# Kernel tuning notes

Measured on AMD Instinct MI355X. Metric: run time of the kernel, lower is better.

The kernel has to match this reference:

```python
import jax, jax.numpy as jnp
import numpy as np

COMMITMENT_COST = 0.25


def setup_inputs() -> dict:
    key = jax.random.key(0)
    k1, k2 = jax.random.split(key)
    B, S, D, K = 8, 4096, 256, 1024
    inputs = jax.random.normal(k1, (B, S, D), dtype=jnp.float32)
    attention_mask = jnp.ones((B, S), dtype=jnp.float32)
    codebook = jax.random.normal(k2, (K, D), dtype=jnp.float32)
    return {"inputs": inputs, "attention_mask": attention_mask, "codebook": codebook}


def reference(inputs, attention_mask, codebook):
    # Inference-mode forward of VectorQuantizer (no EMA update / init / revival).
    B, S, D = inputs.shape
    z = inputs.astype(jnp.float32).reshape(-1, D)          # (N, D)
    m = attention_mask.reshape(-1).astype(jnp.float32)     # (N,)

    cb = codebook.astype(jnp.float32)                      # (K, D)
    # squared L2 distances: ||z||^2 - 2 z e^T + ||e||^2
    dist = (jnp.sum(z * z, axis=-1, keepdims=True)
            - 2.0 * jnp.matmul(z, cb.T)
            + jnp.sum(cb * cb, axis=-1)[None, :])          # (N, K)
    idx = jnp.argmin(dist, axis=-1)                        # (N,)
    q = cb[idx]                                            # (N, D) codebook lookup

    n_valid = jnp.sum(m)
    # mse over valid tokens (elementwise mean, matching F.mse_loss on flat_valid)
    diff = z - jax.lax.stop_gradient(q)
    commitment = jnp.sum(m[:, None] * diff * diff) / (n_valid * D)
    vq_loss = COMMITMENT_COST * commitment

    # straight-through estimator; invalid positions zeroed (as in torch scatter)
    q_ste = z + jax.lax.stop_gradient(q - z)
    quantized = (q_ste * m[:, None]).reshape(B, S, D)
    indices = jnp.where(m > 0, idx, 0).reshape(B, S)
    return quantized, vq_loss, indices
```

## Files before the change

kernel.cpp:

```cpp
#include <hip/hip_runtime.h>
#include <cstdint>

typedef short bf16x8 __attribute__((ext_vector_type(8)));
typedef float f32x16 __attribute__((ext_vector_type(16)));

#define TOK    64
#define CH     64
#define NCH    16
#define BUFW   16384
#define MAXC   32

__device__ __forceinline__ unsigned short f2bf(float f) {
  unsigned u = __float_as_uint(f);
  return (unsigned short)((u + 0x7FFFu + ((u >> 16) & 1u)) >> 16);
}
__device__ __forceinline__ uint4 pack8(float4 a, float4 b) {
  uint4 u;
  u.x = (unsigned)f2bf(a.x) | ((unsigned)f2bf(a.y) << 16);
  u.y = (unsigned)f2bf(a.z) | ((unsigned)f2bf(a.w) << 16);
  u.z = (unsigned)f2bf(b.x) | ((unsigned)f2bf(b.y) << 16);
  u.w = (unsigned)f2bf(b.z) | ((unsigned)f2bf(b.w) << 16);
  return u;
}
__device__ __forceinline__ void gload16(const unsigned short* g, unsigned short* l) {
  __builtin_amdgcn_global_load_lds(
      (const __attribute__((address_space(1))) unsigned int*)(const void*)g,
      (__attribute__((address_space(3))) unsigned int*)(void*)l, 16, 0, 0);
}

__global__ __launch_bounds__(256) void vq_prep(const float* __restrict__ cb,
                                               unsigned short* __restrict__ cb_bf,
                                               float* __restrict__ ee,
                                               float* __restrict__ acc2,
                                               int* __restrict__ done_ctr, int K) {
  if (blockIdx.x == 0 && threadIdx.x == 0) {
    acc2[0] = 0.f; acc2[1] = 0.f; *done_ctr = 0;
  }
  int wave = threadIdx.x >> 6, lane = threadIdx.x & 63;
  int k = blockIdx.x * 4 + wave;
  if (k >= K) return;
  float4 v = *reinterpret_cast<const float4*>(cb + (size_t)k * 256 + lane * 4);
  float s = v.x * v.x + v.y * v.y + v.z * v.z + v.w * v.w;
  #pragma unroll
  for (int off = 32; off; off >>= 1) s += __shfl_down(s, off, 64);
  ushort4 b;
  b.x = f2bf(v.x); b.y = f2bf(v.y); b.z = f2bf(v.z); b.w = f2bf(v.w);
  *reinterpret_cast<ushort4*>(cb_bf + (size_t)k * 256 + lane * 4) = b;
  if (lane == 0) ee[k] = s;
}

__global__ __launch_bounds__(256, 2) void vq_main(
    const float* __restrict__ z, const float* __restrict__ cb,
    const unsigned short* __restrict__ cb_bf, const float* __restrict__ ee,
    const float* __restrict__ mask,
    float* __restrict__ out_q, float* __restrict__ out_idx_f,
    float* __restrict__ out_loss, float* __restrict__ acc2,
    int* __restrict__ done_ctr, int nblocks, int K) {
  __shared__ __align__(16) unsigned short sbuf[2 * BUFW];
  __shared__ float ee_lds[1024];
  __shared__ float znorm[TOK];
  __shared__ int   ccnt[TOK];
  __shared__ unsigned umin[TOK];
  __shared__ unsigned cand[TOK * MAXC];
  __shared__ unsigned short bkbuf[TOK];
  __shared__ float red[8];
  __shared__ bool  last;

  const int t = threadIdx.x;
  const int n0 = blockIdx.x * TOK;
  const int wv = t >> 6, lane = t & 63;
  const int ts = wv & 1, cs = wv >> 1;
  const int l31 = lane & 31, hk = lane >> 5;
  const int q16 = t & 15;

  float ea = ee[t], eb = ee[t + 256], ec = ee[t + 512], ed = ee[t + 768];
  ee_lds[t] = ea; ee_lds[t + 256] = eb; ee_lds[t + 512] = ec; ee_lds[t + 768] = ed;
  if (t < TOK) { ccnt[t] = 0; umin[t] = 0x7F7FFFFFu; }
  float em = fmaxf(fmaxf(ea, eb), fmaxf(ec, ed));
  #pragma unroll
  for (int off = 32; off; off >>= 1) em = fmaxf(em, __shfl_xor(em, off, 64));
  if (lane == 0) red[wv] = em;

  #pragma unroll
  for (int pass = 0; pass < 4; ++pass) {
    int row = pass * 16 + (t >> 4);
    const float* zr = z + (size_t)(n0 + row) * 256;
    float ssq = 0.f;
    #pragma unroll
    for (int j = 0; j < 2; ++j) {
      float4 a = *reinterpret_cast<const float4*>(zr + q16 * 16 + j * 8);
      float4 b = *reinterpret_cast<const float4*>(zr + q16 * 16 + j * 8 + 4);
      ssq += a.x*a.x + a.y*a.y + a.z*a.z + a.w*a.w
           + b.x*b.x + b.y*b.y + b.z*b.z + b.w*b.w;
      int g = q16 * 2 + j;
      *reinterpret_cast<uint4*>(&sbuf[row * 256 + ((g ^ (row & 7)) * 8)]) = pack8(a, b);
    }
    #pragma unroll
    for (int off = 1; off < 16; off <<= 1) ssq += __shfl_xor(ssq, off, 64);
    if (q16 == 0) znorm[row] = sqrtf(ssq);
  }
  __syncthreads();

  const float enmax = sqrtf(fmaxf(fmaxf(red[0], red[1]), fmaxf(red[2], red[3])));

  bf16x8 tfrag[16];
  {
    int row = ts * 32 + l31;
    #pragma unroll
    for (int kk = 0; kk < 16; ++kk) {
      int g = (kk * 2 + hk) ^ (row & 7);
      tfrag[kk] = *reinterpret_cast<const bf16x8*>(&sbuf[row * 256 + g * 8]);
    }
  }
  const float zn = znorm[ts * 32 + l31];
  __syncthreads();

  {
    #pragma unroll
    for (int i = 0; i < 8; ++i) {
      int f = (wv * 8 + i) * 64 + lane;
      int row = f >> 5, slot = f & 31;
      gload16(cb_bf + (size_t)row * 256 + ((slot ^ (row & 7)) * 8),
              &sbuf[(size_t)(wv * 512 + i * 64) * 8]);
    }
  }
  asm volatile("s_waitcnt vmcnt(0)" ::: "memory");
  __syncthreads();

  float am = 3.4e38f;
  const int tok = ts * 32 + l31;

  for (int lc = 0; lc < NCH; ++lc) {
    const int kbase = lc * CH;
    unsigned short* cur = &sbuf[(lc & 1) * BUFW];
    unsigned short* nxt = &sbuf[((lc + 1) & 1) * BUFW];
    if (lc < NCH - 1) {
      const unsigned short* base = cb_bf + (size_t)(kbase + CH) * 256;
      #pragma unroll
      for (int i = 0; i < 8; ++i) {
        int f = (wv * 8 + i) * 64 + lane;
        int row = f >> 5, slot = f & 31;
        gload16(base + (size_t)row * 256 + ((slot ^ (row & 7)) * 8),
                nxt + (size_t)(wv * 512 + i * 64) * 8);
      }
    }

    f32x16 acc = (f32x16){0.f};
    const int arow = cs * 32 + l31;
    const unsigned short* abase = &cur[arow * 256];
    const int asw = arow & 7;
    __builtin_amdgcn_s_setprio(1);
    #pragma unroll
    for (int kk = 0; kk < 16; ++kk) {
      bf16x8 a = *reinterpret_cast<const bf16x8*>(abase + (((kk * 2 + hk) ^ asw) * 8));
      acc = __builtin_amdgcn_mfma_f32_32x32x16_bf16(a, tfrag[kk], acc, 0, 0, 0);
    }
    __builtin_amdgcn_s_setprio(0);

    const int cb0 = kbase + cs * 32 + hk * 4;
    float4 ee4[4];
    #pragma unroll
    for (int gg = 0; gg < 4; ++gg)
      ee4[gg] = *reinterpret_cast<const float4*>(&ee_lds[cb0 + 8 * gg]);

    float dm = 3.4e38f;
    #pragma unroll
    for (int gg = 0; gg < 4; ++gg) {
      float d0 = ee4[gg].x - 2.f * acc[gg * 4 + 0];
      float d1 = ee4[gg].y - 2.f * acc[gg * 4 + 1];
      float d2 = ee4[gg].z - 2.f * acc[gg * 4 + 2];
      float d3 = ee4[gg].w - 2.f * acc[gg * 4 + 3];
      dm = fminf(dm, fminf(fminf(d0, d1), fminf(d2, d3)));
    }
    dm = fmaxf(dm, 0.f);
    atomicMin(&umin[tok], __float_as_uint(dm));
    am = fminf(am, __uint_as_float(umin[tok]));

    if (dm <= am + 1.5f + 0.002f * zn * enmax) {
      #pragma unroll
      for (int gg = 0; gg < 4; ++gg) {
        #pragma unroll
        for (int jj = 0; jj < 4; ++jj) {
          float eej = (jj == 0) ? ee4[gg].x : (jj == 1) ? ee4[gg].y
                    : (jj == 2) ? ee4[gg].z : ee4[gg].w;
          float d = eej - 2.f * acc[gg * 4 + jj];
          if (d <= am + 1.5f + 0.002f * zn * sqrtf(eej)) {
            int code = cb0 + 8 * gg + jj;
            int sl = atomicAdd(&ccnt[tok], 1);
            if (sl < MAXC) cand[tok * MAXC + sl] =
                (__float_as_uint(fmaxf(d, 0.f)) & 0xFFFFFC00u) | (unsigned)code;
          }
        }
      }
    }
    asm volatile("s_waitcnt vmcnt(0)" ::: "memory");
    __syncthreads();
  }

  for (int it = 0; it < 16; ++it) {
    int tk = wv * 16 + it;
    int n = n0 + tk;
    int cnt = ccnt[tk];
    int bk = 0;
    if (cnt > MAXC) {
      float4 zv = *reinterpret_cast<const float4*>(z + (size_t)n * 256 + lane * 4);
      float bs = 3.4e38f;
      for (int k = 0; k < K; k += 2) {
        float4 ca = *reinterpret_cast<const float4*>(cb + (size_t)k * 256 + lane * 4);
        float4 cbv = *reinterpret_cast<const float4*>(cb + (size_t)(k + 1) * 256 + lane * 4);
        float pa = zv.x * ca.x + zv.y * ca.y + zv.z * ca.z + zv.w * ca.w;
        float pb = zv.x * cbv.x + zv.y * cbv.y + zv.z * cbv.z + zv.w * cbv.w;
        #pragma unroll
        for (int off = 32; off; off >>= 1) {
          pa += __shfl_xor(pa, off, 64);
          pb += __shfl_xor(pb, off, 64);
        }
        float sa = ee_lds[k] - 2.f * pa;
        float sb = ee_lds[k + 1] - 2.f * pb;
        if (sa < bs) { bs = sa; bk = k; }
        if (sb < bs) { bs = sb; bk = k + 1; }
      }
    } else {
      float thr = __uint_as_float(umin[tk]) + 1.5f + 0.002f * znorm[tk] * enmax;
      int c = (lane < cnt) ? lane : 0;
      unsigned pe = cand[tk * MAXC + c];
      bool flag = (lane < cnt) && (__uint_as_float(pe & 0xFFFFFC00u) <= thr);
      unsigned long long msk = __ballot(flag);
      if (__popcll(msk) == 1) {
        int cc = __ffsll((long long)msk) - 1;
        bk = (int)(cand[tk * MAXC + cc] & 1023u);
      } else {
        float4 zv = *reinterpret_cast<const float4*>(z + (size_t)n * 256 + lane * 4);
        float bs = 3.4e38f; bk = 1 << 29;
        int cc = 0;
        for (; cc + 4 <= cnt; cc += 4) {
          int k0 = cand[tk * MAXC + cc]     & 1023;
          int k1 = cand[tk * MAXC + cc + 1] & 1023;
          int k2 = cand[tk * MAXC + cc + 2] & 1023;
          int k3 = cand[tk * MAXC + cc + 3] & 1023;
          float4 e0 = *reinterpret_cast<const float4*>(cb + (size_t)k0 * 256 + lane * 4);
          float4 e1 = *reinterpret_cast<const float4*>(cb + (size_t)k1 * 256 + lane * 4);
          float4 e2 = *reinterpret_cast<const float4*>(cb + (size_t)k2 * 256 + lane * 4);
          float4 e3 = *reinterpret_cast<const float4*>(cb + (size_t)k3 * 256 + lane * 4);
          float p0 = zv.x * e0.x + zv.y * e0.y + zv.z * e0.z + zv.w * e0.w;
          float p1 = zv.x * e1.x + zv.y * e1.y + zv.z * e1.z + zv.w * e1.w;
          float p2 = zv.x * e2.x + zv.y * e2.y + zv.z * e2.z + zv.w * e2.w;
          float p3 = zv.x * e3.x + zv.y * e3.y + zv.z * e3.z + zv.w * e3.w;
          #pragma unroll
          for (int off = 32; off; off >>= 1) {
            p0 += __shfl_xor(p0, off, 64);
            p1 += __shfl_xor(p1, off, 64);
            p2 += __shfl_xor(p2, off, 64);
            p3 += __shfl_xor(p3, off, 64);
          }
          float s0 = ee_lds[k0] - 2.f * p0;
          float s1 = ee_lds[k1] - 2.f * p1;
          float s2 = ee_lds[k2] - 2.f * p2;
          float s3 = ee_lds[k3] - 2.f * p3;
          if (s0 < bs || (s0 == bs && k0 < bk)) { bs = s0; bk = k0; }
          if (s1 < bs || (s1 == bs && k1 < bk)) { bs = s1; bk = k1; }
          if (s2 < bs || (s2 == bs && k2 < bk)) { bs = s2; bk = k2; }
          if (s3 < bs || (s3 == bs && k3 < bk)) { bs = s3; bk = k3; }
        }
        for (; cc < cnt; ++cc) {
          int k = cand[tk * MAXC + cc] & 1023;
          float4 ev = *reinterpret_cast<const float4*>(cb + (size_t)k * 256 + lane * 4);
          float dp = zv.x * ev.x + zv.y * ev.y + zv.z * ev.z + zv.w * ev.w;
          #pragma unroll
          for (int off = 32; off; off >>= 1) dp += __shfl_xor(dp, off, 64);
          float s = ee_lds[k] - 2.f * dp;
          if (s < bs || (s == bs && k < bk)) { bs = s; bk = k; }
        }
      }
    }
    bkbuf[tk] = (unsigned short)bk;
  }

  float lsum = 0.f, msum = 0.f;
  for (int it = 0; it < 16; it += 2) {
    int tokA = wv * 16 + it, tokB = tokA + 1;
    int na = n0 + tokA, nb = n0 + tokB;
    int ba = bkbuf[tokA], bb = bkbuf[tokB];
    float4 za = *reinterpret_cast<const float4*>(z + (size_t)na * 256 + lane * 4);
    float4 zb = *reinterpret_cast<const float4*>(z + (size_t)nb * 256 + lane * 4);
    float4 qa = *reinterpret_cast<const float4*>(cb + (size_t)ba * 256 + lane * 4);
    float4 qb = *reinterpret_cast<const float4*>(cb + (size_t)bb * 256 + lane * 4);
    float ma = mask[na], mb = mask[nb];
    float4 oa; oa.x = qa.x * ma; oa.y = qa.y * ma; oa.z = qa.z * ma; oa.w = qa.w * ma;
    float4 ob; ob.x = qb.x * mb; ob.y = qb.y * mb; ob.z = qb.z * mb; ob.w = qb.w * mb;
    *reinterpret_cast<float4*>(out_q + (size_t)na * 256 + lane * 4) = oa;
    *reinterpret_cast<float4*>(out_q + (size_t)nb * 256 + lane * 4) = ob;
    float dxa = za.x - qa.x, dya = za.y - qa.y, dza = za.z - qa.z, dwa = za.w - qa.w;
    float dxb = zb.x - qb.x, dyb = zb.y - qb.y, dzb = zb.z - qb.z, dwb = zb.w - qb.w;
    lsum = fmaf(ma, dxa * dxa + dya * dya + dza * dza + dwa * dwa, lsum);
    lsum = fmaf(mb, dxb * dxb + dyb * dyb + dzb * dzb + dwb * dwb, lsum);
    if (lane == 0) {
      msum += ma + mb;
      out_idx_f[na] = (ma > 0.f) ? (float)ba : 0.f;
      out_idx_f[nb] = (mb > 0.f) ? (float)bb : 0.f;
    }
  }
  #pragma unroll
  for (int off = 32; off; off >>= 1) lsum += __shfl_down(lsum, off, 64);
  if (lane == 0) { red[wv] = lsum; red[4 + wv] = msum; }
  __syncthreads();
  if (t == 0) {
    atomicAdd(&acc2[0], red[0] + red[1] + red[2] + red[3]);
    atomicAdd(&acc2[1], red[4] + red[5] + red[6] + red[7]);
    __threadfence();
    int prev = atomicAdd(done_ctr, 1);
    last = (prev == nblocks - 1);
  }
  __syncthreads();
  if (last && t == 0) {
    float s  = atomicAdd(&acc2[0], 0.0f);
    float nv = atomicAdd(&acc2[1], 0.0f);
    out_loss[0] = (nv > 0.f) ? (0.25f * s / (nv * 256.0f)) : 0.0f;
  }
}

extern "C" void kernel_launch(void* const* d_in, const int* in_sizes, int n_in,
                              void* d_out, int out_size, void* d_ws, size_t ws_size,
                              hipStream_t stream) {
  const float* z    = (const float*)d_in[0];
  const float* mask = (const float*)d_in[1];
  const float* cb   = (const float*)d_in[2];
  const int N = in_sizes[1];
  const int D = 256;
  const int K = in_sizes[2] / D;

  float* wsf  = (float*)d_ws;
  float* acc2 = wsf;
  int*   dctr = (int*)(wsf + 2);
  float* ee   = wsf + 8;
  unsigned short* cb_bf = (unsigned short*)(ee + K);

  float* out_q     = (float*)d_out;
  float* out_loss  = out_q + (size_t)N * D;
  float* out_idx_f = out_loss + 1;

  vq_prep<<<(K + 3) / 4, 256, 0, stream>>>(cb, cb_bf, ee, acc2, dctr, K);
  vq_main<<<N / TOK, 256, 0, stream>>>(z, cb, cb_bf, ee, mask, out_q,
                                       out_idx_f, out_loss, acc2, dctr, N / TOK, K);
}
```

Baseline: 162.2 us.

## Shrink token tile to 32 and switch to 16x16x32 MFMA with global ee reads

```diff
diff --git a/kernel.cpp b/kernel.cpp
--- a/kernel.cpp
+++ b/kernel.cpp
@@ -2,12 +2,12 @@
 #include <cstdint>
 
 typedef short bf16x8 __attribute__((ext_vector_type(8)));
-typedef float f32x16 __attribute__((ext_vector_type(16)));
-
-#define TOK    64
-#define CH     64
-#define NCH    16
-#define BUFW   16384
+typedef float f32x4  __attribute__((ext_vector_type(4)));
+
+#define TOK    32
+#define CH     32
+#define NCH    32
+#define BUFW   8192
 #define MAXC   32
 
 __device__ __forceinline__ unsigned short f2bf(float f) {
@@ -57,7 +57,6 @@
     float* __restrict__ out_loss, float* __restrict__ acc2,
     int* __restrict__ done_ctr, int nblocks, int K) {
   __shared__ __align__(16) unsigned short sbuf[2 * BUFW];
-  __shared__ float ee_lds[1024];
   __shared__ float znorm[TOK];
   __shared__ int   ccnt[TOK];
   __shared__ unsigned umin[TOK];
@@ -70,19 +69,17 @@
   const int n0 = blockIdx.x * TOK;
   const int wv = t >> 6, lane = t & 63;
   const int ts = wv & 1, cs = wv >> 1;
-  const int l31 = lane & 31, hk = lane >> 5;
+  const int quad = lane >> 4, l15 = lane & 15;
   const int q16 = t & 15;
 
-  float ea = ee[t], eb = ee[t + 256], ec = ee[t + 512], ed = ee[t + 768];
-  ee_lds[t] = ea; ee_lds[t + 256] = eb; ee_lds[t + 512] = ec; ee_lds[t + 768] = ed;
   if (t < TOK) { ccnt[t] = 0; umin[t] = 0x7F7FFFFFu; }
-  float em = fmaxf(fmaxf(ea, eb), fmaxf(ec, ed));
+  float em = fmaxf(fmaxf(ee[t], ee[t + 256]), fmaxf(ee[t + 512], ee[t + 768]));
   #pragma unroll
   for (int off = 32; off; off >>= 1) em = fmaxf(em, __shfl_xor(em, off, 64));
   if (lane == 0) red[wv] = em;
 
   #pragma unroll
-  for (int pass = 0; pass < 4; ++pass) {
+  for (int pass = 0; pass < 2; ++pass) {
     int row = pass * 16 + (t >> 4);
     const float* zr = z + (size_t)(n0 + row) * 256;
     float ssq = 0.f;
@@ -103,32 +100,32 @@
 
   const float enmax = sqrtf(fmaxf(fmaxf(red[0], red[1]), fmaxf(red[2], red[3])));
 
-  bf16x8 tfrag[16];
+  bf16x8 tfrag[8];
   {
-    int row = ts * 32 + l31;
-    #pragma unroll
-    for (int kk = 0; kk < 16; ++kk) {
-      int g = (kk * 2 + hk) ^ (row & 7);
+    int row = ts * 16 + l15;
+    #pragma unroll
+    for (int kk = 0; kk < 8; ++kk) {
+      int g = (quad + kk * 4) ^ (row & 7);
       tfrag[kk] = *reinterpret_cast<const bf16x8*>(&sbuf[row * 256 + g * 8]);
     }
   }
-  const float zn = znorm[ts * 32 + l31];
+  const float zn = znorm[ts * 16 + l15];
+  const int tok = ts * 16 + l15;
   __syncthreads();
 
   {
     #pragma unroll
-    for (int i = 0; i < 8; ++i) {
-      int f = (wv * 8 + i) * 64 + lane;
+    for (int i = 0; i < 4; ++i) {
+      int f = (wv * 4 + i) * 64 + lane;
       int row = f >> 5, slot = f & 31;
       gload16(cb_bf + (size_t)row * 256 + ((slot ^ (row & 7)) * 8),
-              &sbuf[(size_t)(wv * 512 + i * 64) * 8]);
+              &sbuf[(size_t)((wv * 4 + i) * 64) * 8]);
     }
   }
   asm volatile("s_waitcnt vmcnt(0)" ::: "memory");
   __syncthreads();
 
   float am = 3.4e38f;
-  const int tok = ts * 32 + l31;
 
   for (int lc = 0; lc < NCH; ++lc) {
     const int kbase = lc * CH;
@@ -137,68 +134,65 @@
     if (lc < NCH - 1) {
       const unsigned short* base = cb_bf + (size_t)(kbase + CH) * 256;
       #pragma unroll
-      for (int i = 0; i < 8; ++i) {
-        int f = (wv * 8 + i) * 64 + lane;
+      for (int i = 0; i < 4; ++i) {
+        int f = (wv * 4 + i) * 64 + lane;
         int row = f >> 5, slot = f & 31;
         gload16(base + (size_t)row * 256 + ((slot ^ (row & 7)) * 8),
-                nxt + (size_t)(wv * 512 + i * 64) * 8);
-      }
-    }
-
-    f32x16 acc = (f32x16){0.f};
-    const int arow = cs * 32 + l31;
+                nxt + (size_t)((wv * 4 + i) * 64) * 8);
+      }
+    }
+
+    const int cb0 = kbase + cs * 16 + quad * 4;
+    float4 ee4 = *reinterpret_cast<const float4*>(&ee[cb0]);
+
+    f32x4 acc = (f32x4){0.f, 0.f, 0.f, 0.f};
+    const int arow = cs * 16 + l15;
     const unsigned short* abase = &cur[arow * 256];
     const int asw = arow & 7;
     __builtin_amdgcn_s_setprio(1);
     #pragma unroll
-    for (int kk = 0; kk < 16; ++kk) {
-      bf16x8 a = *reinterpret_cast<const bf16x8*>(abase + (((kk * 2 + hk) ^ asw) * 8));
-      acc = __builtin_amdgcn_mfma_f32_32x32x16_bf16(a, tfrag[kk], acc, 0, 0, 0);
+    for (int kk = 0; kk < 8; ++kk) {
+      bf16x8 a = *reinterpret_cast<const bf16x8*>(abase + (((quad + kk * 4) ^ asw) * 8));
+      acc = __builtin_amdgcn_mfma_f32_16x16x32_bf16(a, tfrag[kk], acc, 0, 0, 0);
     }
     __builtin_amdgcn_s_setprio(0);
 
-    const int cb0 = kbase + cs * 32 + hk * 4;
-    float4 ee4[4];
-    #pragma unroll
-    for (int gg = 0; gg < 4; ++gg)
-      ee4[gg] = *reinterpret_cast<const float4*>(&ee_lds[cb0 + 8 * gg]);
-
-    float dm = 3.4e38f;
-    #pragma unroll
-    for (int gg = 0; gg < 4; ++gg) {
-      float d0 = ee4[gg].x - 2.f * acc[gg * 4 + 0];
-      float d1 = ee4[gg].y - 2.f * acc[gg * 4 + 1];
-      float d2 = ee4[gg].z - 2.f * acc[gg * 4 + 2];
-      float d3 = ee4[gg].w - 2.f * acc[gg * 4 + 3];
-      dm = fminf(dm, fminf(fminf(d0, d1), fminf(d2, d3)));
-    }
-    dm = fmaxf(dm, 0.f);
+    float d0 = ee4.x - 2.f * acc[0];
+    float d1 = ee4.y - 2.f * acc[1];
+    float d2 = ee4.z - 2.f * acc[2];
+    float d3 = ee4.w - 2.f * acc[3];
+    float dm = fmaxf(fminf(fminf(d0, d1), fminf(d2, d3)), 0.f);
     atomicMin(&umin[tok], __float_as_uint(dm));
     am = fminf(am, __uint_as_float(umin[tok]));
 
     if (dm <= am + 1.5f + 0.002f * zn * enmax) {
-      #pragma unroll
-      for (int gg = 0; gg < 4; ++gg) {
-        #pragma unroll
-        for (int jj = 0; jj < 4; ++jj) {
-          float eej = (jj == 0) ? ee4[gg].x : (jj == 1) ? ee4[gg].y
-                    : (jj == 2) ? ee4[gg].z : ee4[gg].w;
-          float d = eej - 2.f * acc[gg * 4 + jj];
-          if (d <= am + 1.5f + 0.002f * zn * sqrtf(eej)) {
-            int code = cb0 + 8 * gg + jj;
-            int sl = atomicAdd(&ccnt[tok], 1);
-            if (sl < MAXC) cand[tok * MAXC + sl] =
-                (__float_as_uint(fmaxf(d, 0.f)) & 0xFFFFFC00u) | (unsigned)code;
-          }
-        }
+      if (d0 <= am + 1.5f + 0.002f * zn * sqrtf(ee4.x)) {
+        int sl = atomicAdd(&ccnt[tok], 1);
+        if (sl < MAXC) cand[tok * MAXC + sl] =
+            (__float_as_uint(fmaxf(d0, 0.f)) & 0xFFFFFC00u) | (unsigned)(cb0);
+      }
+      if (d1 <= am + 1.5f + 0.002f * zn * sqrtf(ee4.y)) {
+        int sl = atomicAdd(&ccnt[tok], 1);
+        if (sl < MAXC) cand[tok * MAXC + sl] =
+            (__float_as_uint(fmaxf(d1, 0.f)) & 0xFFFFFC00u) | (unsigned)(cb0 + 1);
+      }
+      if (d2 <= am + 1.5f + 0.002f * zn * sqrtf(ee4.z)) {
+        int sl = atomicAdd(&ccnt[tok], 1);
+        if (sl < MAXC) cand[tok * MAXC + sl] =
+            (__float_as_uint(fmaxf(d2, 0.f)) & 0xFFFFFC00u) | (unsigned)(cb0 + 2);
+      }
+      if (d3 <= am + 1.5f + 0.002f * zn * sqrtf(ee4.w)) {
+        int sl = atomicAdd(&ccnt[tok], 1);
+        if (sl < MAXC) cand[tok * MAXC + sl] =
+            (__float_as_uint(fmaxf(d3, 0.f)) & 0xFFFFFC00u) | (unsigned)(cb0 + 3);
       }
     }
     asm volatile("s_waitcnt vmcnt(0)" ::: "memory");
     __syncthreads();
   }
 
-  for (int it = 0; it < 16; ++it) {
-    int tk = wv * 16 + it;
+  for (int it = 0; it < 8; ++it) {
+    int tk = wv * 8 + it;
     int n = n0 + tk;
     int cnt = ccnt[tk];
     int bk = 0;
@@ -215,8 +209,8 @@
           pa += __shfl_xor(pa, off, 64);
           pb += __shfl_xor(pb, off, 64);
         }
-        float sa = ee_lds[k] - 2.f * pa;
-        float sb = ee_lds[k + 1] - 2.f * pb;
+        float sa = ee[k] - 2.f * pa;
+        float sb = ee[k + 1] - 2.f * pb;
         if (sa < bs) { bs = sa; bk = k; }
         if (sb < bs) { bs = sb; bk = k + 1; }
       }
@@ -253,10 +247,10 @@
             p2 += __shfl_xor(p2, off, 64);
             p3 += __shfl_xor(p3, off, 64);
           }
-          float s0 = ee_lds[k0] - 2.f * p0;
-          float s1 = ee_lds[k1] - 2.f * p1;
-          float s2 = ee_lds[k2] - 2.f * p2;
-          float s3 = ee_lds[k3] - 2.f * p3;
+          float s0 = ee[k0] - 2.f * p0;
+          float s1 = ee[k1] - 2.f * p1;
+          float s2 = ee[k2] - 2.f * p2;
+          float s3 = ee[k3] - 2.f * p3;
           if (s0 < bs || (s0 == bs && k0 < bk)) { bs = s0; bk = k0; }
           if (s1 < bs || (s1 == bs && k1 < bk)) { bs = s1; bk = k1; }
           if (s2 < bs || (s2 == bs && k2 < bk)) { bs = s2; bk = k2; }
@@ -268,7 +262,7 @@
           float dp = zv.x * ev.x + zv.y * ev.y + zv.z * ev.z + zv.w * ev.w;
           #pragma unroll
           for (int off = 32; off; off >>= 1) dp += __shfl_xor(dp, off, 64);
-          float s = ee_lds[k] - 2.f * dp;
+          float s = ee[k] - 2.f * dp;
           if (s < bs || (s == bs && k < bk)) { bs = s; bk = k; }
         }
       }
@@ -277,8 +271,8 @@
   }
 
   float lsum = 0.f, msum = 0.f;
-  for (int it = 0; it < 16; it += 2) {
-    int tokA = wv * 16 + it, tokB = tokA + 1;
+  for (int it = 0; it < 8; it += 2) {
+    int tokA = wv * 8 + it, tokB = tokA + 1;
     int na = n0 + tokA, nb = n0 + tokB;
     int ba = bkbuf[tokA], bb = bkbuf[tokB];
     float4 za = *reinterpret_cast<const float4*>(z + (size_t)na * 256 + lane * 4);
```

Result: slower. 216.2 us (+33.3%).
